# Kernel tuning notes

Measured on AMD Instinct MI355X. Metric: run time of the kernel, lower is better.

The kernel has to match this reference:

```python
import jax, jax.numpy as jnp
import numpy as np


def setup_inputs() -> dict:
    key = jax.random.key(0)
    k1, k2, k3, k4 = jax.random.split(key, 4)
    N, D, B = 300000, 256, 512
    x = jax.random.normal(k1, (N, D), dtype=jnp.float32)
    batch = jnp.sort(jax.random.randint(k2, (N,), 0, B, dtype=jnp.int64))
    W1 = jax.random.normal(k3, (D, D // 2), dtype=jnp.float32) / np.sqrt(D)
    b1 = jnp.zeros((D // 2,), dtype=jnp.float32)
    W2 = jax.random.normal(k4, (D // 2, 1), dtype=jnp.float32) / np.sqrt(D // 2)
    b2 = jnp.zeros((1,), dtype=jnp.float32)
    return {"x": x, "batch": batch, "num_segments": B,
            "W1": W1, "b1": b1, "W2": W2, "b2": b2}


def reference(x, batch, num_segments, W1, b1, W2, b2):
    # attention MLP: Linear -> ReLU -> Linear, output [N, 1]
    h = jax.nn.relu(x @ W1 + b1)
    scores = h @ W2 + b2                       # [N, 1]
    # softmax over ALL nodes (dim=0), as in the original module
    w = jax.nn.softmax(scores, axis=0)          # [N, 1]
    # weighted segment-sum per graph; empty segments yield zero rows
    pooled = jax.ops.segment_sum(x * w, batch, num_segments=num_segments)
    return pooled                                # [num_segments, D]
```

## Files before the change

### kernel.cpp

```cpp
#include <hip/hip_runtime.h>
#include <math.h>

typedef __attribute__((ext_vector_type(8))) short bf16x8;
typedef __attribute__((ext_vector_type(4))) float f32x4;

constexpr int D = 256;
constexpr int H = 128;
constexpr int KSTEPS = D / 32;
constexpr int BM = 128;

__device__ __forceinline__ float trunc_bf(float a) {
  return __uint_as_float(__float_as_uint(a) & 0xFFFF0000u);
}
__device__ __forceinline__ unsigned int pack2_bf(float a, float b) {
  return (__float_as_uint(a) >> 16) | (__float_as_uint(b) & 0xFFFF0000u);
}
__device__ __forceinline__ unsigned int pack2_bf_rnd(float a, float b) {
  return ((__float_as_uint(a) + 0x8000u) >> 16) |
         ((__float_as_uint(b) + 0x8000u) & 0xFFFF0000u);
}

union FragU { uint4 u; bf16x8 f; };

__device__ __forceinline__ void gload16(const void* g, void* l) {
  __builtin_amdgcn_global_load_lds(
      (const __attribute__((address_space(1))) unsigned int*)g,
      (__attribute__((address_space(3))) unsigned int*)l, 16, 0, 0);
}
__device__ __forceinline__ void block_sync() {
  asm volatile("" ::: "memory");
  __builtin_amdgcn_s_barrier();
  asm volatile("" ::: "memory");
}

extern "C" __global__ void __launch_bounds__(256)
k_init(float* __restrict__ out, int out_size, float* __restrict__ zacc)
{
  const int i = blockIdx.x * 256 + threadIdx.x;
  if (i < out_size) out[i] = 0.0f;
  if (i == 0) *zacc = 0.0f;
}

extern "C" __global__ void __launch_bounds__(256)
k_pack(const float* __restrict__ W1, uint4* __restrict__ phi,
       uint4* __restrict__ plo)
{
  const int g = blockIdx.x * 256 + threadIdx.x;
  const int c = g >> 9, ht = (g >> 6) & 7, l = g & 63;
  const int kbase = c * 32 + (l >> 4) * 8;
  const int col = ht * 16 + (l & 15);
  float v[8], lo[8];
#pragma unroll
  for (int i = 0; i < 8; ++i) {
    v[i] = W1[(size_t)(kbase + i) * H + col];
    lo[i] = v[i] - trunc_bf(v[i]);
  }
  uint4 h4, l4;
  h4.x = pack2_bf(v[0], v[1]); h4.y = pack2_bf(v[2], v[3]);
  h4.z = pack2_bf(v[4], v[5]); h4.w = pack2_bf(v[6], v[7]);
  l4.x = pack2_bf(lo[0], lo[1]); l4.y = pack2_bf(lo[2], lo[3]);
  l4.z = pack2_bf(lo[4], lo[5]); l4.w = pack2_bf(lo[6], lo[7]);
  phi[g] = h4; plo[g] = l4;
}

extern "C" __global__ void __launch_bounds__(256, 4)
k_fused(const float* __restrict__ x, const int* __restrict__ batch,
        const uint4* __restrict__ phi, const uint4* __restrict__ plo,
        const float* __restrict__ b1, const float* __restrict__ W2,
        const float* __restrict__ b2, float* __restrict__ out,
        float* __restrict__ zacc, int N)
{
  __shared__ float4 xplane[2][1024];
  __shared__ float sred[2][BM];
  __shared__ float wlds[BM];

  const int t = threadIdx.x;
  const int l = t & 63;
  const int w = t >> 6;
  const int lg = l >> 4;
  const int lr = l & 15;
  const int rg = w >> 1;
  const int cg = w & 1;
  const int n0 = blockIdx.x * BM;

  const char* xb = (const char*)x;

  auto STAGE = [&](int buf, int c) {
#pragma unroll
    for (int i = 0; i < 4; ++i) {
      const int plane = i * 4 + w;
      const int g = plane >> 1, p = plane & 1;
      const int srow = min(n0 + g * 16 + lr, N - 1);
      gload16(xb + (size_t)srow * 1024 + c * 128 + lg * 32 + p * 16,
              (char*)&xplane[buf][plane * 64 + l]);
    }
  };

  f32x4 acc[4][4] = {};

  STAGE(0, 0);
#pragma unroll 1
  for (int c = 0; c < KSTEPS; ++c) {
    const int cur = c & 1;
    FragU bhi[4], blo[4];
#pragma unroll
    for (int h = 0; h < 4; ++h) {
      const int ht = cg * 4 + h;
      bhi[h].u = phi[(c * 8 + ht) * 64 + l];
      blo[h].u = plo[(c * 8 + ht) * 64 + l];
    }
    if (c + 1 < KSTEPS) {
      STAGE(cur ^ 1, c + 1);
      asm volatile("s_waitcnt vmcnt(4)" ::: "memory");
    } else {
      asm volatile("s_waitcnt vmcnt(0)" ::: "memory");
    }
    block_sync();

#pragma unroll
    for (int s = 0; s < 4; ++s) {
      const int g = rg * 4 + s;
      const float4 u0 = xplane[cur][(g * 2 + 0) * 64 + l];
      const float4 u1 = xplane[cur][(g * 2 + 1) * 64 + l];
      FragU ahi;
      ahi.u.x = pack2_bf_rnd(u0.x, u0.y);
      ahi.u.y = pack2_bf_rnd(u0.z, u0.w);
      ahi.u.z = pack2_bf_rnd(u1.x, u1.y);
      ahi.u.w = pack2_bf_rnd(u1.z, u1.w);
#pragma unroll
      for (int h = 0; h < 4; ++h) {
        acc[s][h] = __builtin_amdgcn_mfma_f32_16x16x32_bf16(ahi.f, bhi[h].f, acc[s][h], 0, 0, 0);
        acc[s][h] = __builtin_amdgcn_mfma_f32_16x16x32_bf16(ahi.f, blo[h].f, acc[s][h], 0, 0, 0);
      }
    }
    block_sync();
  }

  float bvv[4], wvv[4];
#pragma unroll
  for (int h = 0; h < 4; ++h) {
    const int col = (cg * 4 + h) * 16 + lr;
    bvv[h] = b1[col];
    wvv[h] = W2[col];
  }
#pragma unroll
  for (int s = 0; s < 4; ++s) {
#pragma unroll
    for (int r = 0; r < 4; ++r) {
      float p = 0.0f;
#pragma unroll
      for (int h = 0; h < 4; ++h)
        p = fmaf(fmaxf(acc[s][h][r] + bvv[h], 0.0f), wvv[h], p);
#pragma unroll
      for (int off = 1; off < 16; off <<= 1) p += __shfl_xor(p, off, 64);
      if (lr == 0) sred[cg][rg * 64 + s * 16 + lg * 4 + r] = p;
    }
  }
  __syncthreads();
  if (cg == 0) {
    const int row = rg * 64 + l;
    const int node = n0 + row;
    const float sc = sred[0][row] + sred[1][row] + b2[0];
    const float wgt = (node < N) ? __expf(sc) : 0.0f;
    wlds[row] = wgt;
    float zs = wgt;
#pragma unroll
    for (int off = 1; off < 64; off <<= 1) zs += __shfl_xor(zs, off, 64);
    if (l == 0) atomicAdd(zacc, zs);
  }
  __syncthreads();

  {
    const int nStart = n0 + w * 32;
    const int nEnd = min(nStart + 32, N);
    if (nStart < nEnd) {
      float4 a4 = make_float4(0.f, 0.f, 0.f, 0.f);
      int bprev = batch[nStart];
      for (int n = nStart; n < nEnd; ++n) {
        const int b = batch[n];
        if (b != bprev) {
          float* o = out + (size_t)bprev * D + l * 4;
          atomicAdd(o + 0, a4.x); atomicAdd(o + 1, a4.y);
          atomicAdd(o + 2, a4.z); atomicAdd(o + 3, a4.w);
          a4 = make_float4(0.f, 0.f, 0.f, 0.f);
          bprev = b;
        }
        const float wgt = wlds[n - n0];
        const float4 xv = *reinterpret_cast<const float4*>(x + (size_t)n * D + l * 4);
        a4.x = fmaf(xv.x, wgt, a4.x);
        a4.y = fmaf(xv.y, wgt, a4.y);
        a4.z = fmaf(xv.z, wgt, a4.z);
        a4.w = fmaf(xv.w, wgt, a4.w);
      }
      float* o = out + (size_t)bprev * D + l * 4;
      atomicAdd(o + 0, a4.x); atomicAdd(o + 1, a4.y);
      atomicAdd(o + 2, a4.z); atomicAdd(o + 3, a4.w);
    }
  }
}

extern "C" __global__ void __launch_bounds__(256)
k_finish(float* __restrict__ out, const float* __restrict__ zacc, int size)
{
  const int i = blockIdx.x * 256 + threadIdx.x;
  if (i < size) out[i] *= (1.0f / *zacc);
}

extern "C" void kernel_launch(void* const* d_in, const int* in_sizes, int n_in,
                              void* d_out, int out_size, void* d_ws, size_t ws_size,
                              hipStream_t stream)
{
  const float* x     = (const float*)d_in[0];
  const int*   batch = (const int*)d_in[1];
  const float* W1 = (const float*)d_in[3];
  const float* b1 = (const float*)d_in[4];
  const float* W2 = (const float*)d_in[5];
  const float* b2 = (const float*)d_in[6];
  const int N = in_sizes[1];

  float* zacc = (float*)d_ws;
  uint4* phi  = (uint4*)((char*)d_ws + 256);
  uint4* plo  = (uint4*)((char*)d_ws + 256 + 65536);

  k_init<<<(out_size + 255) / 256, 256, 0, stream>>>((float*)d_out, out_size, zacc);
  k_pack<<<16, 256, 0, stream>>>(W1, phi, plo);

  const int g1 = (N + BM - 1) / BM;
  k_fused<<<g1, 256, 0, stream>>>(x, batch, phi, plo, b1, W2, b2,
                                  (float*)d_out, zacc, N);

  k_finish<<<(out_size + 255) / 256, 256, 0, stream>>>((float*)d_out, zacc, out_size);
}
```

Measured before the change: 170.4 us.

## Switch MLP GEMM from split-bf16 to single fp16 MFMA and halve row tile

```diff
diff --git a/kernel.cpp b/kernel.cpp
--- a/kernel.cpp
+++ b/kernel.cpp
@@ -1,26 +1,22 @@
 #include <hip/hip_runtime.h>
+#include <hip/hip_fp16.h>
 #include <math.h>
 
-typedef __attribute__((ext_vector_type(8))) short bf16x8;
+typedef __attribute__((ext_vector_type(8))) _Float16 f16x8;
+typedef __attribute__((ext_vector_type(2))) __fp16 fp16x2;
 typedef __attribute__((ext_vector_type(4))) float f32x4;
 
 constexpr int D = 256;
 constexpr int H = 128;
 constexpr int KSTEPS = D / 32;
-constexpr int BM = 128;
-
-__device__ __forceinline__ float trunc_bf(float a) {
-  return __uint_as_float(__float_as_uint(a) & 0xFFFF0000u);
-}
-__device__ __forceinline__ unsigned int pack2_bf(float a, float b) {
-  return (__float_as_uint(a) >> 16) | (__float_as_uint(b) & 0xFFFF0000u);
-}
-__device__ __forceinline__ unsigned int pack2_bf_rnd(float a, float b) {
-  return ((__float_as_uint(a) + 0x8000u) >> 16) |
-         ((__float_as_uint(b) + 0x8000u) & 0xFFFF0000u);
-}
-
-union FragU { uint4 u; bf16x8 f; };
+constexpr int BM = 64;
+
+union FragH { uint4 u; f16x8 f; };
+union H2U { fp16x2 h; unsigned int u; };
+
+__device__ __forceinline__ unsigned int pkrtz(float a, float b) {
+  H2U r; r.h = __builtin_amdgcn_cvt_pkrtz(a, b); return r.u;
+}
 
 __device__ __forceinline__ void gload16(const void* g, void* l) {
   __builtin_amdgcn_global_load_lds(
@@ -42,35 +38,34 @@
 }
 
 extern "C" __global__ void __launch_bounds__(256)
-k_pack(const float* __restrict__ W1, uint4* __restrict__ phi,
-       uint4* __restrict__ plo)
+k_pack(const float* __restrict__ W1, uint4* __restrict__ pw)
 {
   const int g = blockIdx.x * 256 + threadIdx.x;
   const int c = g >> 9, ht = (g >> 6) & 7, l = g & 63;
   const int kbase = c * 32 + (l >> 4) * 8;
   const int col = ht * 16 + (l & 15);
-  float v[8], lo[8];
+  unsigned short q[8];
 #pragma unroll
   for (int i = 0; i < 8; ++i) {
-    v[i] = W1[(size_t)(kbase + i) * H + col];
-    lo[i] = v[i] - trunc_bf(v[i]);
-  }
-  uint4 h4, l4;
-  h4.x = pack2_bf(v[0], v[1]); h4.y = pack2_bf(v[2], v[3]);
-  h4.z = pack2_bf(v[4], v[5]); h4.w = pack2_bf(v[6], v[7]);
-  l4.x = pack2_bf(lo[0], lo[1]); l4.y = pack2_bf(lo[2], lo[3]);
-  l4.z = pack2_bf(lo[4], lo[5]); l4.w = pack2_bf(lo[6], lo[7]);
-  phi[g] = h4; plo[g] = l4;
-}
-
-extern "C" __global__ void __launch_bounds__(256, 4)
+    const float v = W1[(size_t)(kbase + i) * H + col];
+    const __half hh = __float2half(v);
+    q[i] = __half_as_ushort(hh);
+  }
+  uint4 h4;
+  h4.x = (unsigned)q[0] | ((unsigned)q[1] << 16);
+  h4.y = (unsigned)q[2] | ((unsigned)q[3] << 16);
+  h4.z = (unsigned)q[4] | ((unsigned)q[5] << 16);
+  h4.w = (unsigned)q[6] | ((unsigned)q[7] << 16);
+  pw[g] = h4;
+}
+
+extern "C" __global__ void __launch_bounds__(256, 6)
 k_fused(const float* __restrict__ x, const int* __restrict__ batch,
-        const uint4* __restrict__ phi, const uint4* __restrict__ plo,
-        const float* __restrict__ b1, const float* __restrict__ W2,
-        const float* __restrict__ b2, float* __restrict__ out,
-        float* __restrict__ zacc, int N)
-{
-  __shared__ float4 xplane[2][1024];
+        const uint4* __restrict__ pw, const float* __restrict__ b1,
+        const float* __restrict__ W2, const float* __restrict__ b2,
+        float* __restrict__ out, float* __restrict__ zacc, int N)
+{
+  __shared__ float4 xplane[2][512];
   __shared__ float sred[2][BM];
   __shared__ float wlds[BM];
 
@@ -87,7 +82,7 @@
 
   auto STAGE = [&](int buf, int c) {
 #pragma unroll
-    for (int i = 0; i < 4; ++i) {
+    for (int i = 0; i < 2; ++i) {
       const int plane = i * 4 + w;
       const int g = plane >> 1, p = plane & 1;
       const int srow = min(n0 + g * 16 + lr, N - 1);
@@ -96,42 +91,37 @@
     }
   };
 
-  f32x4 acc[4][4] = {};
+  f32x4 acc[2][4] = {};
 
   STAGE(0, 0);
 #pragma unroll 1
   for (int c = 0; c < KSTEPS; ++c) {
     const int cur = c & 1;
-    FragU bhi[4], blo[4];
-#pragma unroll
-    for (int h = 0; h < 4; ++h) {
-      const int ht = cg * 4 + h;
-      bhi[h].u = phi[(c * 8 + ht) * 64 + l];
-      blo[h].u = plo[(c * 8 + ht) * 64 + l];
-    }
+    FragH bw[4];
+#pragma unroll
+    for (int h = 0; h < 4; ++h)
+      bw[h].u = pw[(c * 8 + cg * 4 + h) * 64 + l];
     if (c + 1 < KSTEPS) {
       STAGE(cur ^ 1, c + 1);
-      asm volatile("s_waitcnt vmcnt(4)" ::: "memory");
+      asm volatile("s_waitcnt vmcnt(2)" ::: "memory");
     } else {
       asm volatile("s_waitcnt vmcnt(0)" ::: "memory");
     }
     block_sync();
 
 #pragma unroll
-    for (int s = 0; s < 4; ++s) {
-      const int g = rg * 4 + s;
+    for (int s = 0; s < 2; ++s) {
+      const int g = rg * 2 + s;
       const float4 u0 = xplane[cur][(g * 2 + 0) * 64 + l];
       const float4 u1 = xplane[cur][(g * 2 + 1) * 64 + l];
-      FragU ahi;
-      ahi.u.x = pack2_bf_rnd(u0.x, u0.y);
-      ahi.u.y = pack2_bf_rnd(u0.z, u0.w);
-      ahi.u.z = pack2_bf_rnd(u1.x, u1.y);
-      ahi.u.w = pack2_bf_rnd(u1.z, u1.w);
-#pragma unroll
-      for (int h = 0; h < 4; ++h) {
-        acc[s][h] = __builtin_amdgcn_mfma_f32_16x16x32_bf16(ahi.f, bhi[h].f, acc[s][h], 0, 0, 0);
-        acc[s][h] = __builtin_amdgcn_mfma_f32_16x16x32_bf16(ahi.f, blo[h].f, acc[s][h], 0, 0, 0);
-      }
+      FragH a;
+      a.u.x = pkrtz(u0.x, u0.y);
+      a.u.y = pkrtz(u0.z, u0.w);
+      a.u.z = pkrtz(u1.x, u1.y);
+      a.u.w = pkrtz(u1.z, u1.w);
+#pragma unroll
+      for (int h = 0; h < 4; ++h)
+        acc[s][h] = __builtin_amdgcn_mfma_f32_16x16x32_f16(a.f, bw[h].f, acc[s][h], 0, 0, 0);
     }
     block_sync();
   }
@@ -144,7 +134,7 @@
     wvv[h] = W2[col];
   }
 #pragma unroll
-  for (int s = 0; s < 4; ++s) {
+  for (int s = 0; s < 2; ++s) {
 #pragma unroll
     for (int r = 0; r < 4; ++r) {
       float p = 0.0f;
@@ -153,16 +143,16 @@
         p = fmaf(fmaxf(acc[s][h][r] + bvv[h], 0.0f), wvv[h], p);
 #pragma unroll
       for (int off = 1; off < 16; off <<= 1) p += __shfl_xor(p, off, 64);
-      if (lr == 0) sred[cg][rg * 64 + s * 16 + lg * 4 + r] = p;
+      if (lr == 0) sred[cg][rg * 32 + s * 16 + lg * 4 + r] = p;
     }
   }
   __syncthreads();
   if (cg == 0) {
-    const int row = rg * 64 + l;
+    const int row = rg * 32 + (l & 31);
     const int node = n0 + row;
     const float sc = sred[0][row] + sred[1][row] + b2[0];
-    const float wgt = (node < N) ? __expf(sc) : 0.0f;
-    wlds[row] = wgt;
+    const float wgt = (l < 32 && node < N) ? __expf(sc) : 0.0f;
+    if (l < 32) wlds[row] = wgt;
     float zs = wgt;
 #pragma unroll
     for (int off = 1; off < 64; off <<= 1) zs += __shfl_xor(zs, off, 64);
@@ -171,8 +161,8 @@
   __syncthreads();
 
   {
-    const int nStart = n0 + w * 32;
-    const int nEnd = min(nStart + 32, N);
+    const int nStart = n0 + w * 16;
+    const int nEnd = min(nStart + 16, N);
     if (nStart < nEnd) {
       float4 a4 = make_float4(0.f, 0.f, 0.f, 0.f);
       int bprev = batch[nStart];
@@ -219,14 +209,13 @@
   const int N = in_sizes[1];
 
   float* zacc = (float*)d_ws;
-  uint4* phi  = (uint4*)((char*)d_ws + 256);
-  uint4* plo  = (uint4*)((char*)d_ws + 256 + 65536);
+  uint4* pw   = (uint4*)((char*)d_ws + 256);
 
   k_init<<<(out_size + 255) / 256, 256, 0, stream>>>((float*)d_out, out_size, zacc);
-  k_pack<<<16, 256, 0, stream>>>(W1, phi, plo);
+  k_pack<<<16, 256, 0, stream>>>(W1, pw);
 
   const int g1 = (N + BM - 1) / BM;
-  k_fused<<<g1, 256, 0, stream>>>(x, batch, phi, plo, b1, W2, b2,
+  k_fused<<<g1, 256, 0, stream>>>(x, batch, pw, b1, W2, b2,
                                   (float*)d_out, zacc, N);
 
   k_finish<<<(out_size + 255) / 256, 256, 0, stream>>>((float*)d_out, zacc, out_size);
```

Result: slower. 210.6 us (+23.6%).
